# Kernel tuning notes

Hardware: AMD Instinct MI355X
Metric: run time of the kernel (lower is better)

The kernel has to match this reference:

```python
import jax, jax.numpy as jnp
import numpy as np

T_EPS = 1e-07
NUM_CAPSULE = 10
DIM_CAPSULE = 64
ROUTINGS = 5


def squash(x, axis=-1):
    # NOTE: this repo's 'squash' is just norm-division (no s/(1+s) factor)
    s = jnp.sum(x * x, axis=axis, keepdims=True)
    return x / jnp.sqrt(s + T_EPS)


def setup_inputs() -> dict:
    key = jax.random.key(0)
    k1, k2 = jax.random.split(key)
    B, N, D = 128, 512, 300
    M = NUM_CAPSULE * DIM_CAPSULE  # 640
    x = jax.random.normal(k1, (B, N, D), dtype=jnp.float32)
    # xavier_normal for shape (1, D, M): std = sqrt(2/(fan_in+fan_out))
    std = float(np.sqrt(2.0 / (D + M)))
    W = jax.random.normal(k2, (1, D, M), dtype=jnp.float32) * std
    return {"x": x, "W": W}


def reference(x, W):
    B, N, D = x.shape
    # u_hat_vecs: [B, num_capsule(i), input_num_capsule(j), dim_capsule(k)]
    u = jnp.einsum('bnd,dm->bnm', x, W[0])
    u = u.reshape(B, N, NUM_CAPSULE, DIM_CAPSULE).transpose(0, 2, 1, 3)
    b = jnp.zeros((B, NUM_CAPSULE, N), dtype=x.dtype)
    outputs = None
    for i in range(ROUTINGS):
        # softmax over the num_capsule axis (axis=1 of b), matching the
        # permute(0,2,1) -> softmax(dim=2) -> permute back in torch
        c = jax.nn.softmax(b, axis=1)
        outputs = squash(jnp.einsum('bij,bijk->bik', c, u))  # [B, num, dim]
        if i < ROUTINGS - 1:
            b = jnp.einsum('bik,bijk->bij', outputs, u)
    return outputs
```

## Files before the change

kernel.cpp:

```cpp
#include <hip/hip_runtime.h>
#include <hip/hip_bf16.h>
#include <stdint.h>

#define BQ 128
#define NJ 512
#define DD 300
#define NC 10
#define DC 64
#define MM 640
#define KP 320
#define RT 5

typedef __attribute__((ext_vector_type(8))) short short8;
typedef __attribute__((ext_vector_type(4))) float f32x4;


__global__ void k_cast_x(const float* __restrict__ x, __hip_bfloat16* __restrict__ xb) {
    int g = blockIdx.x * 256 + threadIdx.x;
    int row = g / 40, cg2 = g - row * 40;
    const float* src = x + (size_t)row * DD + cg2 * 8;
    float4 a = make_float4(0.f, 0.f, 0.f, 0.f), b4 = a;
    if (cg2 < 37) { a = *(const float4*)src; b4 = *(const float4*)(src + 4); }
    else if (cg2 == 37) { a = *(const float4*)src; }
    union { ushort u[8]; uint4 v; } o;
    float f[8] = {a.x, a.y, a.z, a.w, b4.x, b4.y, b4.z, b4.w};
#pragma unroll
    for (int e = 0; e < 8; ++e) {
        __hip_bfloat16 hh = __float2bfloat16(f[e]);
        o.u[e] = *(ushort*)&hh;
    }
    *(uint4*)(xb + (size_t)row * KP + cg2 * 8) = o.v;
}

__global__ void k_cast_w(const float* __restrict__ w, __hip_bfloat16* __restrict__ wt) {
    int idx = blockIdx.x * 256 + threadIdx.x;
    int m = idx / KP, k = idx - m * KP;
    float v = (k < DD) ? w[(size_t)k * MM + m] : 0.f;
    wt[idx] = __float2bfloat16(v);
}

__global__ void k_zero(float4* __restrict__ p) {
    p[blockIdx.x * 256 + threadIdx.x] = make_float4(0.f, 0.f, 0.f, 0.f);
}


__global__ __launch_bounds__(256)
void k_gemm(const __hip_bfloat16* __restrict__ A,
            const __hip_bfloat16* __restrict__ Bt,
            __hip_bfloat16* __restrict__ C,
            float* __restrict__ su) {
    __shared__ __align__(16) __hip_bfloat16 As[128 * 64];
    __shared__ __align__(16) __hip_bfloat16 Bs[128 * 64];

    const int L  = blockIdx.x;
    const int n0 = ((L >> 3) % 5) * 128;
    const int m0 = ((L / 40) * 8 + (L & 7)) * 128;
    const int t  = threadIdx.x;
    const int w  = t >> 6, lane = t & 63;
    const int wrow = (w >> 1) * 64, wcol = (w & 1) * 64;
    const int quad = lane >> 4, r = lane & 15;

    f32x4 acc[4][4] = {};

    const int srow = t >> 3;
    const int sl   = (t & 7) ^ (srow & 7);
    const __hip_bfloat16* ag = A  + (size_t)(m0 + srow) * KP + sl * 8;
    const __hip_bfloat16* bg = Bt + (size_t)(n0 + srow) * KP + sl * 8;

    for (int kt = 0; kt < KP / 64; ++kt) {
        __syncthreads();
#pragma unroll
        for (int s = 0; s < 4; ++s) {
            __builtin_amdgcn_global_load_lds(
                (const __attribute__((address_space(1))) void*)(ag + (size_t)s * 32 * KP + kt * 64),
                (__attribute__((address_space(3))) void*)(&As[s * 2048 + t * 8]), 16, 0, 0);
            __builtin_amdgcn_global_load_lds(
                (const __attribute__((address_space(1))) void*)(bg + (size_t)s * 32 * KP + kt * 64),
                (__attribute__((address_space(3))) void*)(&Bs[s * 2048 + t * 8]), 16, 0, 0);
        }
        __syncthreads();

#pragma unroll
        for (int hh = 0; hh < 2; ++hh) {
            short8 af[4], bf[4];
#pragma unroll
            for (int mi = 0; mi < 4; ++mi) {
                int rho = wrow + mi * 16 + r;
                int p = (hh * 4 + quad) ^ (rho & 7);
                af[mi] = *(const short8*)&As[rho * 64 + p * 8];
            }
#pragma unroll
            for (int ni = 0; ni < 4; ++ni) {
                int rho = wcol + ni * 16 + r;
                int p = (hh * 4 + quad) ^ (rho & 7);
                bf[ni] = *(const short8*)&Bs[rho * 64 + p * 8];
            }
#pragma unroll
            for (int mi = 0; mi < 4; ++mi)
#pragma unroll
                for (int ni = 0; ni < 4; ++ni)
                    acc[mi][ni] = __builtin_amdgcn_mfma_f32_16x16x32_bf16(
                        af[mi], bf[ni], acc[mi][ni], 0, 0, 0);
        }
    }

#pragma unroll
    for (int mi = 0; mi < 4; ++mi)
#pragma unroll
        for (int ni = 0; ni < 4; ++ni) {
            int col = n0 + wcol + ni * 16 + r;
#pragma unroll
            for (int p = 0; p < 4; ++p) {
                int row = m0 + wrow + mi * 16 + quad * 4 + p;
                C[(size_t)row * MM + col] = __float2bfloat16(acc[mi][ni][p]);
            }
        }

    float cs[4];
#pragma unroll
    for (int ni = 0; ni < 4; ++ni) {
        float s = 0.f;
#pragma unroll
        for (int mi = 0; mi < 4; ++mi)
#pragma unroll
            for (int p = 0; p < 4; ++p) s += acc[mi][ni][p];
        s += __shfl_xor(s, 16, 64);
        s += __shfl_xor(s, 32, 64);
        cs[ni] = s;
    }
    if (quad == 0) {
        int bb = m0 >> 9;
#pragma unroll
        for (int ni = 0; ni < 4; ++ni)
            atomicAdd(&su[(size_t)bb * MM + n0 + wcol + ni * 16 + r], cs[ni]);
    }
}


#define TJ 16
#define NT 8
#define TILE_BYTES (TJ * MM * 2)

__global__ __launch_bounds__(512)
void k_pass(const __hip_bfloat16* __restrict__ u, const float* __restrict__ pprev,
            float* __restrict__ pnext, int first) {
    __shared__ __align__(16) char smem[TILE_BYTES + 32 * 161 * 4 + 160 * 4 + MM * 4];
    ushort* ub    = (ushort*)smem;
    float*  red   = (float*)(smem + TILE_BYTES);
    float*  blj   = (float*)(smem + TILE_BYTES + 20608);
    float*  outl  = (float*)(smem + TILE_BYTES + 20608 + 640);
    float*  pored = (float*)smem;

    const int t   = threadIdx.x;
    const int blk = blockIdx.x;
    const int b   = blk >> 2, q = blk & 3;
    const int w   = t >> 6, lane = t & 63;
    const int jd  = t >> 5, kg = t & 31;

    const char* ubase = (const char*)(u + (size_t)(b * NJ + q * 128) * MM);

    uint4 sa = *(const uint4*)(ubase + t * 16);
    uint4 sb = *(const uint4*)(ubase + 8192 + t * 16);
    uint2 sc = *(const uint2*)(ubase + 16384 + t * 8);

    if (w < 5) {
        float s0, s1;
        if (first) {
            s0 = 0.1f * pprev[(size_t)b * MM + w * 64 + lane];
            s1 = 0.1f * pprev[(size_t)b * MM + 320 + w * 64 + lane];
        } else {
            const float* pp = pprev + (size_t)b * 4 * MM;
            s0 = 0.f; s1 = 0.f;
#pragma unroll
            for (int qq = 0; qq < 4; ++qq) {
                s0 += pp[qq * MM + w * 64 + lane];
                s1 += pp[qq * MM + 320 + w * 64 + lane];
            }
        }
        float q0 = s0 * s0, q1 = s1 * s1;
#pragma unroll
        for (int m = 32; m >= 1; m >>= 1) {
            q0 += __shfl_xor(q0, m, 64);
            q1 += __shfl_xor(q1, m, 64);
        }
        outl[w * 64 + lane]       = s0 * rsqrtf(q0 + 1e-7f);
        outl[320 + w * 64 + lane] = s1 * rsqrtf(q1 + 1e-7f);
    }

    float po[20];
#pragma unroll
    for (int e = 0; e < 20; ++e) po[e] = 0.f;

    for (int tt = 0; tt < NT; ++tt) {
        uint4 na, nb; uint2 nc2;
        if (tt + 1 < NT) {
            const char* ns = ubase + (size_t)(tt + 1) * TILE_BYTES;
            na  = *(const uint4*)(ns + t * 16);
            nb  = *(const uint4*)(ns + 8192 + t * 16);
            nc2 = *(const uint2*)(ns + 16384 + t * 8);
        }
        __syncthreads();
        *(uint4*)((char*)ub + t * 16)        = sa;
        *(uint4*)((char*)ub + 8192 + t * 16) = sb;
        *(uint2*)((char*)ub + 16384 + t * 8) = sc;
        __syncthreads();

        const ushort* urow = ub + jd * MM;
        uint uv[10];
#pragma unroll
        for (int i = 0; i < 10; ++i)
            uv[i] = *(const uint*)(urow + i * 64 + kg * 2);

#pragma unroll
        for (int i = 0; i < 10; ++i) {
            float u0 = __uint_as_float(uv[i] << 16);
            float u1 = __uint_as_float(uv[i] & 0xffff0000u);
            float2 oo = *(const float2*)(outl + i * 64 + kg * 2);
            red[kg * 161 + jd * 10 + i] = u0 * oo.x + u1 * oo.y;
        }
        __syncthreads();
        if (t < 160) {
            float s = 0.f;
#pragma unroll
            for (int g = 0; g < 32; ++g) s += red[g * 161 + t];
            blj[t] = s;
        }
        __syncthreads();
        float c[10];
        {
            float bl[10], mx = -1e30f;
#pragma unroll
            for (int i = 0; i < 10; ++i) { bl[i] = blj[jd * 10 + i]; mx = fmaxf(mx, bl[i]); }
            float ssum = 0.f;
#pragma unroll
            for (int i = 0; i < 10; ++i) { bl[i] = __expf(bl[i] - mx); ssum += bl[i]; }
            float inv = 1.f / ssum;
#pragma unroll
            for (int i = 0; i < 10; ++i) c[i] = bl[i] * inv;
        }
#pragma unroll
        for (int i = 0; i < 10; ++i) {
            float u0 = __uint_as_float(uv[i] << 16);
            float u1 = __uint_as_float(uv[i] & 0xffff0000u);
            po[i * 2 + 0] += c[i] * u0;
            po[i * 2 + 1] += c[i] * u1;
        }
        sa = na; sb = nb; sc = nc2;
    }

#pragma unroll
    for (int e = 0; e < 20; ++e) po[e] += __shfl_xor(po[e], 32, 64);
    __syncthreads();
    if ((t & 63) < 32) {
#pragma unroll
        for (int e = 0; e < 20; ++e) pored[(w * 32 + kg) * 20 + e] = po[e];
    }
    __syncthreads();
    for (int m = t; m < MM; m += 512) {
        int i = m >> 6, k = m & 63, kg2 = k >> 1, kd = k & 1;
        float s = 0.f;
#pragma unroll
        for (int ww = 0; ww < 8; ++ww) s += pored[(ww * 32 + kg2) * 20 + i * 2 + kd];
        pnext[(size_t)blk * MM + m] = s;
    }
}

__global__ __launch_bounds__(640)
void k_squash(const float* __restrict__ pbuf, float* __restrict__ dst) {
    int b = blockIdx.x, t = threadIdx.x;
    float s = 0.f;
#pragma unroll
    for (int qq = 0; qq < 4; ++qq) s += pbuf[(size_t)(b * 4 + qq) * MM + t];
    float sq = s * s;
#pragma unroll
    for (int m = 32; m >= 1; m >>= 1) sq += __shfl_xor(sq, m, 64);
    dst[(size_t)b * MM + t] = s * rsqrtf(sq + 1e-7f);
}


extern "C" void kernel_launch(void* const* d_in, const int* in_sizes, int n_in,
                              void* d_out, int out_size, void* d_ws, size_t ws_size,
                              hipStream_t stream) {
    const float* x = (const float*)d_in[0];
    const float* W = (const float*)d_in[1];
    float* out = (float*)d_out;

    char* ws = (char*)d_ws;
    size_t o = 0;
    __hip_bfloat16* xb = (__hip_bfloat16*)(ws + o); o += (size_t)BQ * NJ * KP * 2;
    __hip_bfloat16* wt = (__hip_bfloat16*)(ws + o); o += (size_t)MM * KP * 2;
    __hip_bfloat16* u  = (__hip_bfloat16*)(ws + o); o += (size_t)BQ * NJ * MM * 2;
    float* pb0 = (float*)(ws + o); o += (size_t)512 * MM * 4;
    float* pb1 = (float*)(ws + o); o += (size_t)512 * MM * 4;
    float* su  = (float*)(ws + o); o += (size_t)BQ * MM * 4;

    k_cast_x<<<(BQ * NJ * 40) / 256, 256, 0, stream>>>(x, xb);
    k_cast_w<<<(MM * KP) / 256, 256, 0, stream>>>(W, wt);
    k_zero<<<(BQ * MM) / (4 * 256), 256, 0, stream>>>((float4*)su);
    k_gemm<<<2560, 256, 0, stream>>>(xb, wt, u, su);

    k_pass<<<512, 512, 0, stream>>>(u, su,  pb0, 1);
    k_pass<<<512, 512, 0, stream>>>(u, pb0, pb1, 0);
    k_pass<<<512, 512, 0, stream>>>(u, pb1, pb0, 0);
    k_pass<<<512, 512, 0, stream>>>(u, pb0, pb1, 0);
    k_squash<<<BQ, 640, 0, stream>>>(pb1, out);
}
```

Baseline: 247.1 us.

## Load routing tiles directly into registers and reduce logits with wave shuffles

The routing pass no longer stages each 16-row u tile through LDS. Each thread now reads its own row slice from global memory straight into registers, with the next tile prefetched. The per-row agreement logits are reduced with cross-lane xor shuffles inside 32-lane groups, which replaces the LDS scratch array plus two block barriers per tile. This removes most __syncthreads and LDS traffic, at the cost of narrower 4-byte global loads and more register pressure.

```diff
diff --git a/kernel.cpp b/kernel.cpp
--- a/kernel.cpp
+++ b/kernel.cpp
@@ -137,19 +137,11 @@
 }
 
 
-#define TJ 16
-#define NT 8
-#define TILE_BYTES (TJ * MM * 2)
-
 __global__ __launch_bounds__(512)
 void k_pass(const __hip_bfloat16* __restrict__ u, const float* __restrict__ pprev,
             float* __restrict__ pnext, int first) {
-    __shared__ __align__(16) char smem[TILE_BYTES + 32 * 161 * 4 + 160 * 4 + MM * 4];
-    ushort* ub    = (ushort*)smem;
-    float*  red   = (float*)(smem + TILE_BYTES);
-    float*  blj   = (float*)(smem + TILE_BYTES + 20608);
-    float*  outl  = (float*)(smem + TILE_BYTES + 20608 + 640);
-    float*  pored = (float*)smem;
+    __shared__ __align__(16) float outl[MM];
+    __shared__ __align__(16) float pored[8 * 32 * 20];
 
     const int t   = threadIdx.x;
     const int blk = blockIdx.x;
@@ -157,11 +149,12 @@
     const int w   = t >> 6, lane = t & 63;
     const int jd  = t >> 5, kg = t & 31;
 
-    const char* ubase = (const char*)(u + (size_t)(b * NJ + q * 128) * MM);
-
-    uint4 sa = *(const uint4*)(ubase + t * 16);
-    uint4 sb = *(const uint4*)(ubase + 8192 + t * 16);
-    uint2 sc = *(const uint2*)(ubase + 16384 + t * 8);
+    const ushort* ubase = (const ushort*)u
+        + (size_t)(b * NJ + q * 128 + jd) * MM + kg * 2;
+
+    uint uv[10];
+#pragma unroll
+    for (int i = 0; i < 10; ++i) uv[i] = *(const uint*)(ubase + i * 64);
 
     if (w < 5) {
         float s0, s1;
@@ -186,72 +179,62 @@
         outl[w * 64 + lane]       = s0 * rsqrtf(q0 + 1e-7f);
         outl[320 + w * 64 + lane] = s1 * rsqrtf(q1 + 1e-7f);
     }
+    __syncthreads();
+
+    float2 oo[10];
+#pragma unroll
+    for (int i = 0; i < 10; ++i) oo[i] = *(const float2*)(&outl[i * 64 + kg * 2]);
 
     float po[20];
 #pragma unroll
     for (int e = 0; e < 20; ++e) po[e] = 0.f;
 
-    for (int tt = 0; tt < NT; ++tt) {
-        uint4 na, nb; uint2 nc2;
-        if (tt + 1 < NT) {
-            const char* ns = ubase + (size_t)(tt + 1) * TILE_BYTES;
-            na  = *(const uint4*)(ns + t * 16);
-            nb  = *(const uint4*)(ns + 8192 + t * 16);
-            nc2 = *(const uint2*)(ns + 16384 + t * 8);
-        }
-        __syncthreads();
-        *(uint4*)((char*)ub + t * 16)        = sa;
-        *(uint4*)((char*)ub + 8192 + t * 16) = sb;
-        *(uint2*)((char*)ub + 16384 + t * 8) = sc;
-        __syncthreads();
-
-        const ushort* urow = ub + jd * MM;
-        uint uv[10];
-#pragma unroll
-        for (int i = 0; i < 10; ++i)
-            uv[i] = *(const uint*)(urow + i * 64 + kg * 2);
-
+    for (int tt = 0; tt < 8; ++tt) {
+        uint nv[10];
+        if (tt < 7) {
+            const ushort* nrow = ubase + (size_t)(tt + 1) * 16 * MM;
+#pragma unroll
+            for (int i = 0; i < 10; ++i) nv[i] = *(const uint*)(nrow + i * 64);
+        }
+
+        float bl[10];
 #pragma unroll
         for (int i = 0; i < 10; ++i) {
             float u0 = __uint_as_float(uv[i] << 16);
             float u1 = __uint_as_float(uv[i] & 0xffff0000u);
-            float2 oo = *(const float2*)(outl + i * 64 + kg * 2);
-            red[kg * 161 + jd * 10 + i] = u0 * oo.x + u1 * oo.y;
-        }
-        __syncthreads();
-        if (t < 160) {
-            float s = 0.f;
-#pragma unroll
-            for (int g = 0; g < 32; ++g) s += red[g * 161 + t];
-            blj[t] = s;
-        }
-        __syncthreads();
-        float c[10];
-        {
-            float bl[10], mx = -1e30f;
-#pragma unroll
-            for (int i = 0; i < 10; ++i) { bl[i] = blj[jd * 10 + i]; mx = fmaxf(mx, bl[i]); }
-            float ssum = 0.f;
-#pragma unroll
-            for (int i = 0; i < 10; ++i) { bl[i] = __expf(bl[i] - mx); ssum += bl[i]; }
-            float inv = 1.f / ssum;
-#pragma unroll
-            for (int i = 0; i < 10; ++i) c[i] = bl[i] * inv;
-        }
+            bl[i] = u0 * oo[i].x + u1 * oo[i].y;
+        }
+#pragma unroll
+        for (int m = 1; m <= 16; m <<= 1)
+#pragma unroll
+            for (int i = 0; i < 10; ++i) bl[i] += __shfl_xor(bl[i], m, 64);
+
+        float mx = -1e30f;
+#pragma unroll
+        for (int i = 0; i < 10; ++i) mx = fmaxf(mx, bl[i]);
+        float ssum = 0.f;
+#pragma unroll
+        for (int i = 0; i < 10; ++i) { bl[i] = __expf(bl[i] - mx); ssum += bl[i]; }
+        float inv = 1.f / ssum;
+
 #pragma unroll
         for (int i = 0; i < 10; ++i) {
+            float cc = bl[i] * inv;
             float u0 = __uint_as_float(uv[i] << 16);
             float u1 = __uint_as_float(uv[i] & 0xffff0000u);
-            po[i * 2 + 0] += c[i] * u0;
-            po[i * 2 + 1] += c[i] * u1;
-        }
-        sa = na; sb = nb; sc = nc2;
+            po[i * 2 + 0] += cc * u0;
+            po[i * 2 + 1] += cc * u1;
+        }
+
+        if (tt < 7) {
+#pragma unroll
+            for (int i = 0; i < 10; ++i) uv[i] = nv[i];
+        }
     }
 
 #pragma unroll
     for (int e = 0; e < 20; ++e) po[e] += __shfl_xor(po[e], 32, 64);
-    __syncthreads();
-    if ((t & 63) < 32) {
+    if (lane < 32) {
 #pragma unroll
         for (int e = 0; e < 20; ++e) pored[(w * 32 + kg) * 20 + e] = po[e];
     }
```

Result: slower. 255.1 us (+3.2%).
